# Kernel optimization log

Measured on AMD Instinct MI355X. Metric: run time of the kernel, lower is better.

The kernel has to match this reference:

```python
import jax, jax.numpy as jnp
import numpy as np

NUM_CLASSES = 5
B, D, H, W = 4, 64, 256, 256


def _per_class_counts(labels, weights, num_classes):
    # labels: [B, N] int, weights: [B, N] float -> [B, C] float counts
    b = labels.shape[0]
    ids = labels + jnp.arange(b, dtype=labels.dtype)[:, None] * num_classes
    counts = jax.ops.segment_sum(weights.ravel(), ids.ravel().astype(jnp.int32),
                                 num_segments=b * num_classes)
    return counts.reshape(b, num_classes)


def _dice(predicted, target, num_classes):
    b = predicted.shape[0]
    p = predicted.reshape(b, -1)  # [B, N] integer class labels
    t = target.reshape(b, -1)
    ones = jnp.ones(p.shape, dtype=jnp.float32)
    pred_sum = _per_class_counts(p, ones, num_classes)                      # sum of one-hot(pred) over voxels
    tar_sum = _per_class_counts(t, ones, num_classes)                       # sum of one-hot(target) over voxels
    inter = _per_class_counts(p, (p == t).astype(jnp.float32), num_classes) # per-class intersection counts
    num = 2.0 * inter
    den = pred_sum + tar_sum
    zero = den == 0
    num = jnp.where(zero, 1.0, num)
    den = jnp.where(zero, 1.0, den)
    return (num / den).mean(axis=0)  # [C]


def setup_inputs() -> dict:
    key = jax.random.key(0)
    k1, k2 = jax.random.split(key)
    predicted = jax.random.randint(k1, (B, D, H, W), 0, NUM_CLASSES, dtype=jnp.int32)
    target = jax.random.randint(k2, (B, D, H, W), 0, NUM_CLASSES, dtype=jnp.int32)
    return {"predicted": predicted, "target": target}


def reference(predicted, target):
    return _dice(predicted, target, NUM_CLASSES)
```

## Files before the change

### kernel.cpp

```cpp
#include <hip/hip_runtime.h>

#define NUM_CLASSES 5
#define BATCH 4
#define NPB (64 * 256 * 256)
#define VEC_PER_BATCH (NPB / 4)
#define THREADS 256
#define VECS 16
#define BLOCKS_X (VEC_PER_BATCH / (THREADS * VECS))
#define SLOTS 15
#define PSTRIDE 16


typedef int v4i __attribute__((ext_vector_type(4)));

#define GLOAD(Q, VOFF, SBASE) \
  asm volatile("global_load_dwordx4 %0, %1, %2" : "=v"(Q) : "v"(VOFF), "s"(SBASE))

#define WAITP(N, P, T) \
  asm volatile("s_waitcnt vmcnt(" #N ")" : "+v"(P), "+v"(T))

__global__ __launch_bounds__(THREADS, 4) void dice_count_kernel(
    const int* __restrict__ pred, const int* __restrict__ targ,
    unsigned int* __restrict__ partial) {
  const int b = blockIdx.y;
  const unsigned long long pB = (unsigned long long)(
      pred + (long long)b * NPB + (long long)blockIdx.x * (THREADS * VECS * 4));
  const unsigned long long tB = (unsigned long long)(
      targ + (long long)b * NPB + (long long)blockIdx.x * (THREADS * VECS * 4));

  unsigned vo[VECS];
#pragma unroll
  for (int k = 0; k < VECS; ++k) vo[k] = threadIdx.x * 16u + (unsigned)k * 4096u;

  v4i qp[VECS], qt[VECS];

  unsigned accP0 = 0, accP1 = 0, accT0 = 0, accT1 = 0, accI0 = 0, accI1 = 0;

#define ACC_ELEM(PE, TE, AP, AT, AI)                   \
    {                                                  \
      const unsigned op = 1u << (6u * (unsigned)(PE)); \
      AP += op;                                        \
      AT += 1u << (6u * (unsigned)(TE));               \
      AI += ((PE) == (TE)) ? op : 0u;                  \
    }
#define CONS1(PV, TV, AP, AT, AI)                      \
    ACC_ELEM(PV[0], TV[0], AP, AT, AI)                 \
    ACC_ELEM(PV[1], TV[1], AP, AT, AI)                 \
    ACC_ELEM(PV[2], TV[2], AP, AT, AI)                 \
    ACC_ELEM(PV[3], TV[3], AP, AT, AI)

#define ISSUE(K)  GLOAD(qp[K], vo[K], pB); GLOAD(qt[K], vo[K], tB)
#define STEP(K, N, AP, AT, AI) \
    WAITP(N, qp[K], qt[K]);    \
    CONS1(qp[K], qt[K], AP, AT, AI)

  ISSUE(0); ISSUE(1); ISSUE(2); ISSUE(3);
  ISSUE(4); ISSUE(5); ISSUE(6); ISSUE(7);
  STEP(0, 14, accP0, accT0, accI0); ISSUE(8);
  STEP(1, 14, accP0, accT0, accI0); ISSUE(9);
  STEP(2, 14, accP0, accT0, accI0); ISSUE(10);
  STEP(3, 14, accP0, accT0, accI0); ISSUE(11);
  STEP(4, 14, accP0, accT0, accI0); ISSUE(12);
  STEP(5, 14, accP0, accT0, accI0); ISSUE(13);
  STEP(6, 14, accP0, accT0, accI0); ISSUE(14);
  STEP(7, 14, accP0, accT0, accI0); ISSUE(15);
  STEP(8,  14, accP1, accT1, accI1);
  STEP(9,  12, accP1, accT1, accI1);
  STEP(10, 10, accP1, accT1, accI1);
  STEP(11,  8, accP1, accT1, accI1);
  STEP(12,  6, accP1, accT1, accI1);
  STEP(13,  4, accP1, accT1, accI1);
  STEP(14,  2, accP1, accT1, accI1);
  STEP(15,  0, accP1, accT1, accI1);

#define UNPACK(A0, A1, R01, R23, R4)                                     \
  unsigned R01 = ((A0 & 63u) + (A1 & 63u)) |                             \
                 ((((A0 >> 6) & 63u) + ((A1 >> 6) & 63u)) << 16);        \
  unsigned R23 = (((A0 >> 12) & 63u) + ((A1 >> 12) & 63u)) |             \
                 ((((A0 >> 18) & 63u) + ((A1 >> 18) & 63u)) << 16);      \
  unsigned R4 = ((A0 >> 24) & 63u) + ((A1 >> 24) & 63u);
  UNPACK(accP0, accP1, p01, p23, p4r)
  UNPACK(accT0, accT1, t01, t23, t4r)
  UNPACK(accI0, accI1, i01, i23, i4r)

#pragma unroll
  for (int off = 32; off >= 1; off >>= 1) {
    p01 += (unsigned)__shfl_xor((int)p01, off);
    p23 += (unsigned)__shfl_xor((int)p23, off);
    p4r += (unsigned)__shfl_xor((int)p4r, off);
    t01 += (unsigned)__shfl_xor((int)t01, off);
    t23 += (unsigned)__shfl_xor((int)t23, off);
    t4r += (unsigned)__shfl_xor((int)t4r, off);
    i01 += (unsigned)__shfl_xor((int)i01, off);
    i23 += (unsigned)__shfl_xor((int)i23, off);
    i4r += (unsigned)__shfl_xor((int)i4r, off);
  }

  __shared__ unsigned int s[SLOTS];
  if (threadIdx.x < SLOTS) s[threadIdx.x] = 0;
  __syncthreads();

  if ((threadIdx.x & 63) == 0) {
    atomicAdd(&s[0], p01 & 0xFFFFu);
    atomicAdd(&s[1], p01 >> 16);
    atomicAdd(&s[2], p23 & 0xFFFFu);
    atomicAdd(&s[3], p23 >> 16);
    atomicAdd(&s[4], p4r);
    atomicAdd(&s[5], t01 & 0xFFFFu);
    atomicAdd(&s[6], t01 >> 16);
    atomicAdd(&s[7], t23 & 0xFFFFu);
    atomicAdd(&s[8], t23 >> 16);
    atomicAdd(&s[9], t4r);
    atomicAdd(&s[10], i01 & 0xFFFFu);
    atomicAdd(&s[11], i01 >> 16);
    atomicAdd(&s[12], i23 & 0xFFFFu);
    atomicAdd(&s[13], i23 >> 16);
    atomicAdd(&s[14], i4r);
  }
  __syncthreads();

  if (threadIdx.x < SLOTS)
    partial[(b * BLOCKS_X + blockIdx.x) * PSTRIDE + threadIdx.x] = s[threadIdx.x];
}

__global__ __launch_bounds__(256) void dice_final_kernel(
    const unsigned int* __restrict__ partial, float* __restrict__ out) {
  __shared__ unsigned int red[BATCH * SLOTS][4];
  const int t = threadIdx.x;
  if (t < BATCH * SLOTS * 4) {
    const int q = t & 3;
    const int s = (t >> 2) % SLOTS;
    const int bb = (t >> 2) / SLOTS;
    unsigned int sum = 0;
    for (int j = q * (BLOCKS_X / 4); j < (q + 1) * (BLOCKS_X / 4); ++j)
      sum += partial[(bb * BLOCKS_X + j) * PSTRIDE + s];
    red[(t >> 2)][q] = sum;
  }
  __syncthreads();
  if (t < NUM_CLASSES) {
    float acc = 0.0f;
#pragma unroll
    for (int bb = 0; bb < BATCH; ++bb) {
      const int ip = bb * SLOTS + t;
      const int it = bb * SLOTS + 5 + t;
      const int ii = bb * SLOTS + 10 + t;
      const float ps = (float)(red[ip][0] + red[ip][1] + red[ip][2] + red[ip][3]);
      const float ts = (float)(red[it][0] + red[it][1] + red[it][2] + red[it][3]);
      const float is = (float)(red[ii][0] + red[ii][1] + red[ii][2] + red[ii][3]);
      float num = 2.0f * is;
      float den = ps + ts;
      if (den == 0.0f) { num = 1.0f; den = 1.0f; }
      acc += num / den;
    }
    out[t] = acc * (1.0f / BATCH);
  }
}

extern "C" void kernel_launch(void* const* d_in, const int* in_sizes, int n_in,
                              void* d_out, int out_size, void* d_ws, size_t ws_size,
                              hipStream_t stream) {
  const int* pred = (const int*)d_in[0];
  const int* targ = (const int*)d_in[1];
  float* out = (float*)d_out;
  unsigned int* partial = (unsigned int*)d_ws;

  dim3 grid(BLOCKS_X, BATCH);
  dice_count_kernel<<<grid, THREADS, 0, stream>>>(pred, targ, partial);
  dice_final_kernel<<<1, 256, 0, stream>>>(partial, out);
}
```

Before: 150.4 us.

## Use four rotating load buffers instead of sixteen in dice count kernel

Replaces the sixteen per-iteration register buffers with four rotating buffers, so each thread keeps at most four pairs of dwordx4 loads in flight instead of eight. This cuts vector register use per thread. The launch-bounds occupancy hint also drops from 4 to 2 blocks per CU. The trade is less memory-level parallelism per wave, which has to be made up by more resident waves for this bandwidth-bound kernel.

```diff
diff --git a/kernel.cpp b/kernel.cpp
--- a/kernel.cpp
+++ b/kernel.cpp
@@ -19,7 +19,7 @@
 #define WAITP(N, P, T) \
   asm volatile("s_waitcnt vmcnt(" #N ")" : "+v"(P), "+v"(T))
 
-__global__ __launch_bounds__(THREADS, 4) void dice_count_kernel(
+__global__ __launch_bounds__(THREADS, 2) void dice_count_kernel(
     const int* __restrict__ pred, const int* __restrict__ targ,
     unsigned int* __restrict__ partial) {
   const int b = blockIdx.y;
@@ -28,11 +28,9 @@
   const unsigned long long tB = (unsigned long long)(
       targ + (long long)b * NPB + (long long)blockIdx.x * (THREADS * VECS * 4));
 
-  unsigned vo[VECS];
-#pragma unroll
-  for (int k = 0; k < VECS; ++k) vo[k] = threadIdx.x * 16u + (unsigned)k * 4096u;
+  const unsigned vo0 = threadIdx.x * 16u;
 
-  v4i qp[VECS], qt[VECS];
+  v4i pr0, pr1, pr2, pr3, tr0, tr1, tr2, tr3;
 
   unsigned accP0 = 0, accP1 = 0, accT0 = 0, accT1 = 0, accI0 = 0, accI1 = 0;
 
@@ -49,29 +47,30 @@
     ACC_ELEM(PV[2], TV[2], AP, AT, AI)                 \
     ACC_ELEM(PV[3], TV[3], AP, AT, AI)
 
-#define ISSUE(K)  GLOAD(qp[K], vo[K], pB); GLOAD(qt[K], vo[K], tB)
-#define STEP(K, N, AP, AT, AI) \
-    WAITP(N, qp[K], qt[K]);    \
-    CONS1(qp[K], qt[K], AP, AT, AI)
+#define ISSUE(BUF, K) \
+    GLOAD(pr##BUF, vo0 + (K) * 4096u, pB); \
+    GLOAD(tr##BUF, vo0 + (K) * 4096u, tB)
+#define STEP(BUF, N, AP, AT, AI) \
+    WAITP(N, pr##BUF, tr##BUF);  \
+    CONS1(pr##BUF, tr##BUF, AP, AT, AI)
 
-  ISSUE(0); ISSUE(1); ISSUE(2); ISSUE(3);
-  ISSUE(4); ISSUE(5); ISSUE(6); ISSUE(7);
-  STEP(0, 14, accP0, accT0, accI0); ISSUE(8);
-  STEP(1, 14, accP0, accT0, accI0); ISSUE(9);
-  STEP(2, 14, accP0, accT0, accI0); ISSUE(10);
-  STEP(3, 14, accP0, accT0, accI0); ISSUE(11);
-  STEP(4, 14, accP0, accT0, accI0); ISSUE(12);
-  STEP(5, 14, accP0, accT0, accI0); ISSUE(13);
-  STEP(6, 14, accP0, accT0, accI0); ISSUE(14);
-  STEP(7, 14, accP0, accT0, accI0); ISSUE(15);
-  STEP(8,  14, accP1, accT1, accI1);
-  STEP(9,  12, accP1, accT1, accI1);
-  STEP(10, 10, accP1, accT1, accI1);
-  STEP(11,  8, accP1, accT1, accI1);
-  STEP(12,  6, accP1, accT1, accI1);
-  STEP(13,  4, accP1, accT1, accI1);
-  STEP(14,  2, accP1, accT1, accI1);
-  STEP(15,  0, accP1, accT1, accI1);
+  ISSUE(0, 0); ISSUE(1, 1); ISSUE(2, 2); ISSUE(3, 3);
+  STEP(0, 6, accP0, accT0, accI0); ISSUE(0, 4);
+  STEP(1, 6, accP0, accT0, accI0); ISSUE(1, 5);
+  STEP(2, 6, accP0, accT0, accI0); ISSUE(2, 6);
+  STEP(3, 6, accP0, accT0, accI0); ISSUE(3, 7);
+  STEP(0, 6, accP0, accT0, accI0); ISSUE(0, 8);
+  STEP(1, 6, accP0, accT0, accI0); ISSUE(1, 9);
+  STEP(2, 6, accP0, accT0, accI0); ISSUE(2, 10);
+  STEP(3, 6, accP0, accT0, accI0); ISSUE(3, 11);
+  STEP(0, 6, accP1, accT1, accI1); ISSUE(0, 12);
+  STEP(1, 6, accP1, accT1, accI1); ISSUE(1, 13);
+  STEP(2, 6, accP1, accT1, accI1); ISSUE(2, 14);
+  STEP(3, 6, accP1, accT1, accI1); ISSUE(3, 15);
+  STEP(0, 6, accP1, accT1, accI1);
+  STEP(1, 4, accP1, accT1, accI1);
+  STEP(2, 2, accP1, accT1, accI1);
+  STEP(3, 0, accP1, accT1, accI1);
 
 #define UNPACK(A0, A1, R01, R23, R4)                                     \
   unsigned R01 = ((A0 & 63u) + (A1 & 63u)) |                             \
```

After: 149.5 us. No clear change (-0.6%).

## Stage loads through LDS with direct global-to-LDS async copies in a ring

Applied to the files above, without the earlier changes.

Replaces the 16-deep register-held global_load_dwordx4 prefetch with global_load_lds copies into a per-wave 4-slot LDS ring. Each wave waits on vmcnt, reads its slot from LDS, then refills that slot. The aim is to cut VGPR pressure and keep loads streaming through an explicit software pipeline. The cost is a much shallower in-flight depth per thread, extra LDS reads, 32KB of LDS per block, and a possible race between LDS reads and the next async write into the same slot.

```diff
diff --git a/kernel.cpp b/kernel.cpp
--- a/kernel.cpp
+++ b/kernel.cpp
@@ -9,32 +9,41 @@
 #define BLOCKS_X (VEC_PER_BATCH / (THREADS * VECS))
 #define SLOTS 15
 #define PSTRIDE 16
+#define DEPTH 4
 
 
 typedef int v4i __attribute__((ext_vector_type(4)));
 
-#define GLOAD(Q, VOFF, SBASE) \
-  asm volatile("global_load_dwordx4 %0, %1, %2" : "=v"(Q) : "v"(VOFF), "s"(SBASE))
+__device__ __forceinline__ void gload_lds16(const int* gp, int* lp) {
+  __builtin_amdgcn_global_load_lds(
+      (const __attribute__((address_space(1))) void*)gp,
+      (__attribute__((address_space(3))) void*)lp, 16, 0, 0);
+}
 
-#define WAITP(N, P, T) \
-  asm volatile("s_waitcnt vmcnt(" #N ")" : "+v"(P), "+v"(T))
+#define WAITN(N) asm volatile("s_waitcnt vmcnt(" #N ")" ::: "memory")
 
 __global__ __launch_bounds__(THREADS, 4) void dice_count_kernel(
     const int* __restrict__ pred, const int* __restrict__ targ,
     unsigned int* __restrict__ partial) {
   const int b = blockIdx.y;
-  const unsigned long long pB = (unsigned long long)(
-      pred + (long long)b * NPB + (long long)blockIdx.x * (THREADS * VECS * 4));
-  const unsigned long long tB = (unsigned long long)(
-      targ + (long long)b * NPB + (long long)blockIdx.x * (THREADS * VECS * 4));
+  const int tid = threadIdx.x;
+  const int w = tid >> 6;
+  const int lane = tid & 63;
 
-  unsigned vo[VECS];
-#pragma unroll
-  for (int k = 0; k < VECS; ++k) vo[k] = threadIdx.x * 16u + (unsigned)k * 4096u;
+  const int* pB = pred + (long long)b * NPB +
+                  (long long)blockIdx.x * (THREADS * VECS * 4);
+  const int* tB = targ + (long long)b * NPB +
+                  (long long)blockIdx.x * (THREADS * VECS * 4);
 
-  v4i qp[VECS], qt[VECS];
+  __shared__ int stage[4][DEPTH][2][256];
 
   unsigned accP0 = 0, accP1 = 0, accT0 = 0, accT1 = 0, accI0 = 0, accI1 = 0;
+
+#define STAGE(R)                                                        \
+  gload_lds16(pB + ((R) * THREADS + tid) * 4,                           \
+              &stage[w][(R) & (DEPTH - 1)][0][0]);                      \
+  gload_lds16(tB + ((R) * THREADS + tid) * 4,                           \
+              &stage[w][(R) & (DEPTH - 1)][1][0]);
 
 #define ACC_ELEM(PE, TE, AP, AT, AI)                   \
     {                                                  \
@@ -43,35 +52,41 @@
       AT += 1u << (6u * (unsigned)(TE));               \
       AI += ((PE) == (TE)) ? op : 0u;                  \
     }
-#define CONS1(PV, TV, AP, AT, AI)                      \
-    ACC_ELEM(PV[0], TV[0], AP, AT, AI)                 \
-    ACC_ELEM(PV[1], TV[1], AP, AT, AI)                 \
-    ACC_ELEM(PV[2], TV[2], AP, AT, AI)                 \
-    ACC_ELEM(PV[3], TV[3], AP, AT, AI)
 
-#define ISSUE(K)  GLOAD(qp[K], vo[K], pB); GLOAD(qt[K], vo[K], tB)
-#define STEP(K, N, AP, AT, AI) \
-    WAITP(N, qp[K], qt[K]);    \
-    CONS1(qp[K], qt[K], AP, AT, AI)
+#define CONSUME(R, AP, AT, AI)                                          \
+  {                                                                     \
+    const v4i pv = *(const v4i*)&stage[w][(R) & (DEPTH - 1)][0][lane * 4]; \
+    const v4i tv = *(const v4i*)&stage[w][(R) & (DEPTH - 1)][1][lane * 4]; \
+    ACC_ELEM(pv[0], tv[0], AP, AT, AI)                                  \
+    ACC_ELEM(pv[1], tv[1], AP, AT, AI)                                  \
+    ACC_ELEM(pv[2], tv[2], AP, AT, AI)                                  \
+    ACC_ELEM(pv[3], tv[3], AP, AT, AI)                                  \
+  }
 
-  ISSUE(0); ISSUE(1); ISSUE(2); ISSUE(3);
-  ISSUE(4); ISSUE(5); ISSUE(6); ISSUE(7);
-  STEP(0, 14, accP0, accT0, accI0); ISSUE(8);
-  STEP(1, 14, accP0, accT0, accI0); ISSUE(9);
-  STEP(2, 14, accP0, accT0, accI0); ISSUE(10);
-  STEP(3, 14, accP0, accT0, accI0); ISSUE(11);
-  STEP(4, 14, accP0, accT0, accI0); ISSUE(12);
-  STEP(5, 14, accP0, accT0, accI0); ISSUE(13);
-  STEP(6, 14, accP0, accT0, accI0); ISSUE(14);
-  STEP(7, 14, accP0, accT0, accI0); ISSUE(15);
-  STEP(8,  14, accP1, accT1, accI1);
-  STEP(9,  12, accP1, accT1, accI1);
-  STEP(10, 10, accP1, accT1, accI1);
-  STEP(11,  8, accP1, accT1, accI1);
-  STEP(12,  6, accP1, accT1, accI1);
-  STEP(13,  4, accP1, accT1, accI1);
-  STEP(14,  2, accP1, accT1, accI1);
-  STEP(15,  0, accP1, accT1, accI1);
+  STAGE(0) STAGE(1) STAGE(2) STAGE(3)
+
+#define STEP(R, AP, AT, AI)                      \
+  WAITN(6);                                      \
+  CONSUME(R, AP, AT, AI)                         \
+  __builtin_amdgcn_sched_barrier(0);             \
+  STAGE(R + 4)
+
+  STEP(0, accP0, accT0, accI0)
+  STEP(1, accP0, accT0, accI0)
+  STEP(2, accP0, accT0, accI0)
+  STEP(3, accP0, accT0, accI0)
+  STEP(4, accP0, accT0, accI0)
+  STEP(5, accP0, accT0, accI0)
+  STEP(6, accP0, accT0, accI0)
+  STEP(7, accP0, accT0, accI0)
+  STEP(8, accP1, accT1, accI1)
+  STEP(9, accP1, accT1, accI1)
+  STEP(10, accP1, accT1, accI1)
+  STEP(11, accP1, accT1, accI1)
+  WAITN(6); CONSUME(12, accP1, accT1, accI1)
+  WAITN(4); CONSUME(13, accP1, accT1, accI1)
+  WAITN(2); CONSUME(14, accP1, accT1, accI1)
+  WAITN(0); CONSUME(15, accP1, accT1, accI1)
 
 #define UNPACK(A0, A1, R01, R23, R4)                                     \
   unsigned R01 = ((A0 & 63u) + (A1 & 63u)) |                             \
```

After: 149.4 us. Within noise of the previous version (-0.7%).
